# Optimization experiments

Measured on AMD Instinct MI355X. Metric: run time of the kernel, lower is better.

## Reference

```python
import jax, jax.numpy as jnp
import numpy as np

N = 4096     # num nodes
FEAT = 500   # knn attribute dim
HID = 512    # args.hid_dim
E = 65536    # edges (avg degree 16)
T = 8        # args.time -> euler steps with step_size=1


def setup_inputs() -> dict:
    key = jax.random.key(0)
    ks = jax.random.split(key, 10)
    knn = jax.random.normal(ks[0], (N, FEAT), jnp.float32)
    adj = jax.random.uniform(ks[1], (N, N), jnp.float32)
    norm_factor = jnp.ones((), jnp.float32)
    edge_index = jax.random.randint(ks[2], (2, E), 0, N, dtype=jnp.int32).astype(jnp.int64)
    edge_weight = jax.random.uniform(ks[3], (E,), jnp.float32)
    # AGCN params (init eye + small noise so math is non-trivial)
    w1 = jnp.eye(N, dtype=jnp.float32) + 0.01 * jax.random.normal(ks[4], (N, N), jnp.float32)
    w2 = jnp.eye(N, dtype=jnp.float32) + 0.01 * jax.random.normal(ks[5], (N, N), jnp.float32)
    # extractor: Linear(N, HID) then Linear(HID, HID), kaiming-normal (relu), zero bias
    W0 = jax.random.normal(ks[6], (HID, N), jnp.float32) * np.float32((2.0 / N) ** 0.5)
    b0 = jnp.zeros((HID,), jnp.float32)
    W1 = jax.random.normal(ks[7], (HID, HID), jnp.float32) * np.float32((2.0 / HID) ** 0.5)
    b1 = jnp.zeros((HID,), jnp.float32)
    # LaplacianODEFunc scalar params
    alpha_train = jnp.asarray(0.5, jnp.float32)
    beta_train = jnp.asarray(0.1, jnp.float32)
    return dict(knn=knn, adj=adj, norm_factor=norm_factor, w1=w1, w2=w2,
                W0=W0, b0=b0, W1=W1, b1=b1, edge_weight=edge_weight,
                alpha_train=alpha_train, beta_train=beta_train, edge_index=edge_index)


def _spmm(edge_index, edge_weight, x):
    # out[row] += w * x[col], row=edge_index[0], col=edge_index[1]
    msg = edge_weight[:, None] * x[edge_index[1]]          # [E, HID]
    return jax.ops.segment_sum(msg, edge_index[0], num_segments=x.shape[0])


def reference(knn, adj, norm_factor, w1, w2, W0, b0, W1, b1,
              edge_weight, alpha_train, beta_train, edge_index):
    # ---- AGCN ----
    H = (adj @ w1) @ adj.T                                  # [N, N]
    H = (H @ w2) @ knn                                      # [N, FEAT]
    embed = H @ H.T                                         # [N, N]
    norm = jnp.maximum(jnp.linalg.norm(embed, axis=1, keepdims=True), 1e-12)
    embed = embed / norm                                    # F.normalize(dim=1)
    # ---- extractor MLP (no activation in source; dropout=eval no-op) ----
    h = embed @ W0.T + b0                                   # [N, HID]
    h = h @ W1.T + b1                                       # [N, HID]
    # ---- ODE diffusion: dx/dt = sigmoid(a)*(Ax - x) + b*x0, explicit Euler dt=1 ----
    x0 = jax.lax.stop_gradient(h)
    alpha = jax.nn.sigmoid(alpha_train)

    def step(x, _):
        ax = _spmm(edge_index, edge_weight, x)
        return x + alpha * (ax - x) + beta_train * x0, None

    z_ode, _ = jax.lax.scan(step, h, None, length=T)
    z = jax.nn.relu(norm_factor * z_ode + h)
    z = (z - z.mean(0)) / jnp.std(z, ddof=1)                # torch std is unbiased
    return z
```

## Files before the change

### kernel.cpp

```cpp
#include <hip/hip_runtime.h>
#include <stdint.h>
#include <stddef.h>

typedef __bf16 bf16;
typedef __attribute__((ext_vector_type(8))) __bf16 bf16x8;
typedef __attribute__((ext_vector_type(4))) __bf16 bf16x4;
typedef __attribute__((ext_vector_type(4))) float f32x4;

#define NN 4096
#define HIDD 512
#define NE 65536

__device__ inline void gll16(const void* g, void* l) {
    __builtin_amdgcn_global_load_lds(
        (const __attribute__((address_space(1))) void*)g,
        (__attribute__((address_space(3))) void*)l, 16, 0, 0);
}

__global__ void cvt_f32_bf16(const float* __restrict__ in, bf16* __restrict__ out, int n) {
    int i = (blockIdx.x * 256 + threadIdx.x) * 4;
    if (i >= n) return;
    float4 v = *reinterpret_cast<const float4*>(in + i);
    bf16x4 o;
    o[0] = (bf16)v.x; o[1] = (bf16)v.y; o[2] = (bf16)v.z; o[3] = (bf16)v.w;
    *reinterpret_cast<bf16x4*>(out + i) = o;
}

__global__ void reduce_bf16_slices(const bf16* __restrict__ in, bf16* __restrict__ out,
                                   int n, int S) {
    int i = (blockIdx.x * 256 + threadIdx.x) * 8;
    if (i >= n) return;
    float acc[8] = {};
    for (int k = 0; k < S; ++k) {
        bf16x8 v = *reinterpret_cast<const bf16x8*>(in + (size_t)k * n + i);
#pragma unroll
        for (int j = 0; j < 8; ++j) acc[j] += (float)v[j];
    }
    bf16x8 o;
#pragma unroll
    for (int j = 0; j < 8; ++j) o[j] = (bf16)acc[j];
    *reinterpret_cast<bf16x8*>(out + i) = o;
}

__global__ void transpose_pad_f32(const float* __restrict__ in, bf16* __restrict__ out,
                                  int R, int C, int Cpad) {
    __shared__ bf16 tile[32][33];
    int c0 = blockIdx.x * 32, r0 = blockIdx.y * 32;
    int tx = threadIdx.x, ty = threadIdx.y;
    for (int i = ty; i < 32; i += 8) {
        int r = r0 + i, c = c0 + tx;
        bf16 v = (bf16)0.f;
        if (r < R && c < C) v = (bf16)in[(size_t)r * C + c];
        tile[i][tx] = v;
    }
    __syncthreads();
    for (int i = ty; i < 32; i += 8) {
        int oc = c0 + i, orow = r0 + tx;
        if (oc < Cpad && orow < R) out[(size_t)oc * R + orow] = tile[tx][i];
    }
}

__global__ void transpose_dual_f32(const float* __restrict__ in, bf16* __restrict__ outT,
                                   bf16* __restrict__ outD, int Nn) {
    __shared__ bf16 tile[32][33];
    int c0 = blockIdx.x * 32, r0 = blockIdx.y * 32;
    int tx = threadIdx.x, ty = threadIdx.y;
    for (int i = ty; i < 32; i += 8) {
        int r = r0 + i, c = c0 + tx;
        bf16 v = (bf16)in[(size_t)r * Nn + c];
        tile[i][tx] = v;
        outD[(size_t)r * Nn + c] = v;
    }
    __syncthreads();
    for (int i = ty; i < 32; i += 8)
        outT[(size_t)(c0 + i) * Nn + r0 + tx] = tile[tx][i];
}

__global__ void transpose_bf16(const bf16* __restrict__ in, bf16* __restrict__ out,
                               int R, int C) {
    __shared__ bf16 tile[32][33];
    int c0 = blockIdx.x * 32, r0 = blockIdx.y * 32;
    int tx = threadIdx.x, ty = threadIdx.y;
    for (int i = ty; i < 32; i += 8)
        tile[i][tx] = in[(size_t)(r0 + i) * C + c0 + tx];
    __syncthreads();
    for (int i = ty; i < 32; i += 8)
        out[(size_t)(c0 + i) * R + r0 + tx] = tile[tx][i];
}

template<int OMODE, bool HAS_BIAS, bool ROW_SCALE>
__global__ __launch_bounds__(256)
void gemm_nt(const bf16* __restrict__ A, const bf16* __restrict__ B,
             void* __restrict__ Cp, const float* __restrict__ bias,
             const float* __restrict__ rowscale, int M, int N, int K) {
    __shared__ __align__(16) bf16 As[128 * 32];
    __shared__ __align__(16) bf16 Bs[128 * 32];
    const int tid  = threadIdx.x;
    const int wave = tid >> 6;
    const int lane = tid & 63;
    const int m0 = blockIdx.y * 128, n0 = blockIdx.x * 128;
    const int lrow = lane >> 2;
    const int lcol = (lane & 3) * 8;
    const int c0 = wave * 2;
    const size_t arow0 = (size_t)(m0 + c0 * 16 + lrow) * K + lcol;
    const size_t arow1 = (size_t)(m0 + (c0 + 1) * 16 + lrow) * K + lcol;
    const size_t brow0 = (size_t)(n0 + c0 * 16 + lrow) * K + lcol;
    const size_t brow1 = (size_t)(n0 + (c0 + 1) * 16 + lrow) * K + lcol;
    bf16* asd0 = &As[c0 * 512];
    bf16* asd1 = &As[(c0 + 1) * 512];
    bf16* bsd0 = &Bs[c0 * 512];
    bf16* bsd1 = &Bs[(c0 + 1) * 512];

    f32x4 acc[4][4] = {};

    const int wm = (wave >> 1) * 64;
    const int wn = (wave & 1) * 64;
    const int fm = wm + (lane & 15);
    const int fn = wn + (lane & 15);
    const int fk = (lane >> 4) * 8;

    const int kper = K / gridDim.z;
    const int kz0 = blockIdx.z * kper;
    const int kz1 = kz0 + kper;

    for (int k0 = kz0; k0 < kz1; k0 += 32) {
        gll16(A + arow0 + k0, asd0);
        gll16(A + arow1 + k0, asd1);
        gll16(B + brow0 + k0, bsd0);
        gll16(B + brow1 + k0, bsd1);
        __syncthreads();
        bf16x8 af[4], bg[4];
#pragma unroll
        for (int i = 0; i < 4; ++i)
            af[i] = *reinterpret_cast<const bf16x8*>(&As[(fm + i * 16) * 32 + fk]);
#pragma unroll
        for (int j = 0; j < 4; ++j)
            bg[j] = *reinterpret_cast<const bf16x8*>(&Bs[(fn + j * 16) * 32 + fk]);
#pragma unroll
        for (int i = 0; i < 4; ++i)
#pragma unroll
            for (int j = 0; j < 4; ++j)
                acc[i][j] = __builtin_amdgcn_mfma_f32_16x16x32_bf16(af[i], bg[j], acc[i][j], 0, 0, 0);
        __syncthreads();
    }

    const int rbase = m0 + wm + (lane >> 4) * 4;
    const int cbase = n0 + wn + (lane & 15);
    float* outf = (float*)Cp + (size_t)blockIdx.z * M * N;
    bf16*  outb = (bf16*)Cp;
    bf16*  outp = (bf16*)Cp + (size_t)blockIdx.z * M * N;
#pragma unroll
    for (int i = 0; i < 4; ++i) {
#pragma unroll
        for (int j = 0; j < 4; ++j) {
            int col = cbase + j * 16;
            float bv = 0.f;
            if (HAS_BIAS) bv = bias[col];
#pragma unroll
            for (int r = 0; r < 4; ++r) {
                int row = rbase + i * 16 + r;
                float v = acc[i][j][r];
                if (ROW_SCALE) v *= rowscale[row];
                v += bv;
                if (OMODE == 0)      outf[(size_t)row * N + col] = v;
                else if (OMODE == 1) outb[(size_t)row * N + col] = (bf16)v;
                else                 outp[(size_t)row * N + col] = (bf16)v;
            }
        }
    }
}

__global__ void colnorm_part(const bf16* __restrict__ Ht, const float* __restrict__ Rf,
                             float* __restrict__ n2) {
    int i = blockIdx.x * 128 + threadIdx.x;
    int a0 = blockIdx.y * 64;
    const float* Rf2 = Rf + (size_t)HIDD * NN;
    float s = 0.f;
    for (int a = a0; a < a0 + 64; ++a) {
        size_t idx = (size_t)a * NN + i;
        s += (Rf[idx] + Rf2[idx]) * (float)Ht[idx];
    }
    atomicAdd(&n2[i], s);
}

__global__ void colnorm_fin(const float* __restrict__ n2, float* __restrict__ inv) {
    int i = blockIdx.x * 256 + threadIdx.x;
    inv[i] = 1.f / fmaxf(sqrtf(n2[i]), 1e-12f);
}

__global__ void bias_fuse(const float* __restrict__ W1, const float* __restrict__ b0,
                          const float* __restrict__ b1, float* __restrict__ bp) {
    int row = blockIdx.x * 4 + (threadIdx.x >> 6);
    int lane = threadIdx.x & 63;
    const float4* wr = (const float4*)(W1 + (size_t)row * HIDD);
    const float4* bz = (const float4*)b0;
    float s = 0.f;
#pragma unroll
    for (int j = 0; j < 2; ++j) {
        float4 a = wr[lane * 2 + j], b = bz[lane * 2 + j];
        s += a.x * b.x + a.y * b.y + a.z * b.z + a.w * b.w;
    }
    for (int off = 32; off; off >>= 1) s += __shfl_down(s, off);
    if (lane == 0) bp[row] = b1[row] + s;
}

__global__ void reduce2_scale_bias(const bf16* __restrict__ p, bf16* __restrict__ out,
                                   const float* __restrict__ inv, const float* __restrict__ bp) {
    int i = (blockIdx.x * 256 + threadIdx.x) * 8;
    const int n = NN * HIDD;
    bf16x8 a = *reinterpret_cast<const bf16x8*>(p + i);
    bf16x8 b = *reinterpret_cast<const bf16x8*>(p + n + i);
    int row = i >> 9;
    int col = i & (HIDD - 1);
    float sc = inv[row];
    bf16x8 o;
#pragma unroll
    for (int j = 0; j < 8; ++j)
        o[j] = (bf16)(((float)a[j] + (float)b[j]) * sc + bp[col + j]);
    *reinterpret_cast<bf16x8*>(out + i) = o;
}

__global__ void csr_count(const int* __restrict__ ei, int* __restrict__ cnt, int E) {
    int e = blockIdx.x * 256 + threadIdx.x;
    if (e < E) atomicAdd(&cnt[ei[e]], 1);
}

__global__ void scan_4096(const int* __restrict__ cnt, int* __restrict__ rs) {
    __shared__ int s[1024];
    int t = threadIdx.x;
    int b = t * 4;
    int a0 = cnt[b], a1 = cnt[b + 1], a2 = cnt[b + 2], a3 = cnt[b + 3];
    int tot = a0 + a1 + a2 + a3;
    s[t] = tot;
    __syncthreads();
    for (int off = 1; off < 1024; off <<= 1) {
        int v = (t >= off) ? s[t - off] : 0;
        __syncthreads();
        s[t] += v;
        __syncthreads();
    }
    int excl = s[t] - tot;
    rs[b] = excl; rs[b + 1] = excl + a0; rs[b + 2] = excl + a0 + a1; rs[b + 3] = excl + a0 + a1 + a2;
    if (t == 1023) rs[4096] = s[1023];
}

__global__ void csr_scatter(const int* __restrict__ ei, const float* __restrict__ ew,
                            int* __restrict__ cur, int* __restrict__ ccol,
                            float* __restrict__ cw, int E) {
    int e = blockIdx.x * 256 + threadIdx.x;
    if (e < E) {
        int r = ei[e];
        int p = atomicAdd(&cur[r], 1);
        ccol[p] = ei[E + e];
        cw[p] = ew[e];
    }
}

__global__ void ode_step_bf16(const bf16* __restrict__ xin, const bf16* __restrict__ x0,
                              bf16* __restrict__ xout, const int* __restrict__ rs,
                              const int* __restrict__ ccol, const float* __restrict__ cw,
                              const float* __restrict__ alpha_p, const float* __restrict__ beta_p) {
    int row = blockIdx.x * 4 + (threadIdx.x >> 6);
    int lane = threadIdx.x & 63;
    float alpha = 1.f / (1.f + expf(-alpha_p[0]));
    float beta = beta_p[0];
    const bf16x8* xin8 = (const bf16x8*)xin;
    float acc[8] = {};
    int p0 = rs[row], p1 = rs[row + 1];
    for (int p = p0; p < p1; ++p) {
        int c = ccol[p]; float w = cw[p];
        bf16x8 v = xin8[(size_t)c * 64 + lane];
#pragma unroll
        for (int j = 0; j < 8; ++j) acc[j] += w * (float)v[j];
    }
    bf16x8 xi = xin8[(size_t)row * 64 + lane];
    bf16x8 xz = ((const bf16x8*)x0)[(size_t)row * 64 + lane];
    bf16x8 r;
#pragma unroll
    for (int j = 0; j < 8; ++j) {
        float x = (float)xi[j];
        r[j] = (bf16)(x + alpha * (acc[j] - x) + beta * (float)xz[j]);
    }
    ((bf16x8*)xout)[(size_t)row * 64 + lane] = r;
}

__global__ void epi1(const bf16* __restrict__ x8, const bf16* __restrict__ h,
                     const float* __restrict__ nf_p, float* __restrict__ z,
                     float* __restrict__ colsum, float* __restrict__ gst) {
    __shared__ float r1[512], r2[512];
    int b = blockIdx.x, j = threadIdx.x;
    float nf = nf_p[0];
    float cp = 0.f, sq = 0.f;
    for (int i = 0; i < 8; ++i) {
        size_t idx = (size_t)(b * 8 + i) * HIDD + j;
        float v = nf * (float)x8[idx] + (float)h[idx];
        v = fmaxf(v, 0.f);
        z[idx] = v;
        cp += v; sq += v * v;
    }
    atomicAdd(&colsum[j], cp);
    r1[j] = cp; r2[j] = sq;
    __syncthreads();
    for (int off = 256; off > 0; off >>= 1) {
        if (j < off) { r1[j] += r1[j + off]; r2[j] += r2[j + off]; }
        __syncthreads();
    }
    if (j == 0) { atomicAdd(&gst[0], r1[0]); atomicAdd(&gst[1], r2[0]); }
}

__global__ void epi2(const float* __restrict__ z, const float* __restrict__ colsum,
                     const float* __restrict__ gst, float* __restrict__ out) {
    size_t idx = (size_t)blockIdx.x * 256 + threadIdx.x;
    int j = (int)(idx & (HIDD - 1));
    float n = (float)NN * (float)HIDD;
    float gmean = gst[0] / n;
    float var = (gst[1] - n * gmean * gmean) / (n - 1.f);
    float istd = rsqrtf(var);
    float mean = colsum[j] * (1.f / (float)NN);
    out[idx] = (z[idx] - mean) * istd;
}

extern "C" void kernel_launch(void* const* d_in, const int* in_sizes, int n_in,
                              void* d_out, int out_size, void* d_ws, size_t ws_size,
                              hipStream_t stream) {
    const float* knn  = (const float*)d_in[0];
    const float* adj  = (const float*)d_in[1];
    const float* nf   = (const float*)d_in[2];
    const float* w1   = (const float*)d_in[3];
    const float* w2   = (const float*)d_in[4];
    const float* W0   = (const float*)d_in[5];
    const float* b0   = (const float*)d_in[6];
    const float* W1   = (const float*)d_in[7];
    const float* b1   = (const float*)d_in[8];
    const float* ew   = (const float*)d_in[9];
    const float* alph = (const float*)d_in[10];
    const float* beta = (const float*)d_in[11];
    const int*   ei   = (const int*)d_in[12];

    char* w = (char*)d_ws;
    size_t off = 0;
    auto alloc = [&](size_t bytes) -> char* {
        char* p = w + off;
        off += (bytes + 255) & ~(size_t)255;
        return p;
    };
    const size_t SZ_NN  = (size_t)NN * NN * sizeof(bf16);
    const size_t SZ_TH  = (size_t)HIDD * NN * sizeof(bf16);
    bf16* Bar  = (bf16*)alloc(SZ_NN);
    bf16* Car  = (bf16*)alloc(SZ_NN);
    bf16* Adjb = (bf16*)alloc(SZ_NN);
    bf16* knnT = (bf16*)alloc(SZ_TH);
    bf16* tA   = (bf16*)alloc(SZ_TH);
    bf16* tB   = (bf16*)alloc(SZ_TH);
    float* tf  = (float*)alloc((size_t)32 * 1024 * 1024);
    bf16* Hm   = (bf16*)alloc(SZ_TH);
    bf16* Gb   = (bf16*)alloc((size_t)HIDD * HIDD * sizeof(bf16));
    bf16* M0b  = (bf16*)alloc((size_t)HIDD * HIDD * sizeof(bf16));
    bf16* Qtb  = (bf16*)alloc((size_t)HIDD * HIDD * sizeof(bf16));
    bf16* hb   = (bf16*)alloc((size_t)NN * HIDD * sizeof(bf16));
    float* inv = (float*)alloc(NN * sizeof(float));
    float* n2  = (float*)alloc(NN * sizeof(float));
    int*  cnt  = (int*)alloc(NN * sizeof(int));
    int*  rs   = (int*)alloc((NN + 1) * sizeof(int));
    int*  cur  = (int*)alloc(NN * sizeof(int));
    int*  ccol = (int*)alloc(NE * sizeof(int));
    float* cw  = (float*)alloc(NE * sizeof(float));
    float* colsum = (float*)alloc(HIDD * sizeof(float));
    float* gst = (float*)alloc(2 * sizeof(float));
    float* bp  = (float*)alloc(HIDD * sizeof(float));
    bf16* tfb = (bf16*)tf;
    bf16* W1b = (bf16*)((char*)Car + 16 * 1024 * 1024);
    bf16* xA  = (bf16*)Car;
    bf16* xB  = (bf16*)Car + (size_t)NN * HIDD;
    (void)ws_size; (void)n_in; (void)in_sizes; (void)out_size;

    dim3 tb(32, 8);
    const int nTH = HIDD * NN;
    const int nHH = HIDD * HIDD;

    transpose_pad_f32<<<dim3(16, 128), tb, 0, stream>>>(knn, knnT, NN, 500, HIDD);
    cvt_f32_bf16<<<(NN * NN) / 1024, 256, 0, stream>>>(w2, Car, NN * NN);
    transpose_dual_f32<<<dim3(128, 128), tb, 0, stream>>>(adj, Bar, Adjb, NN);

    gemm_nt<2, false, false><<<dim3(32, 4, 8), 256, 0, stream>>>(knnT, Car, tfb, nullptr, nullptr, HIDD, NN, NN);
    reduce_bf16_slices<<<nTH / 2048, 256, 0, stream>>>(tfb, tA, nTH, 8);
    gemm_nt<2, false, false><<<dim3(32, 4, 8), 256, 0, stream>>>(tA, Bar, tfb, nullptr, nullptr, HIDD, NN, NN);
    reduce_bf16_slices<<<nTH / 2048, 256, 0, stream>>>(tfb, tB, nTH, 8);
    cvt_f32_bf16<<<(NN * NN) / 1024, 256, 0, stream>>>(w1, Car, NN * NN);
    gemm_nt<2, false, false><<<dim3(32, 4, 8), 256, 0, stream>>>(tB, Car, tfb, nullptr, nullptr, HIDD, NN, NN);
    reduce_bf16_slices<<<nTH / 2048, 256, 0, stream>>>(tfb, tA, nTH, 8);
    gemm_nt<2, false, false><<<dim3(32, 4, 8), 256, 0, stream>>>(tA, Adjb, tfb, nullptr, nullptr, HIDD, NN, NN);
    reduce_bf16_slices<<<nTH / 2048, 256, 0, stream>>>(tfb, tB, nTH, 8);

    transpose_bf16<<<dim3(128, 16), tb, 0, stream>>>(tB, Hm, HIDD, NN);

    gemm_nt<2, false, false><<<dim3(4, 4, 32), 256, 0, stream>>>(tB, tB, tfb, nullptr, nullptr, HIDD, HIDD, NN);
    reduce_bf16_slices<<<nHH / 2048, 256, 0, stream>>>(tfb, Gb, nHH, 32);

    gemm_nt<0, false, false><<<dim3(32, 4, 2), 256, 0, stream>>>(Gb, Hm, tf, nullptr, nullptr, HIDD, NN, HIDD);
    hipMemsetAsync(n2, 0, NN * sizeof(float), stream);
    colnorm_part<<<dim3(32, 8), 128, 0, stream>>>(tB, tf, n2);
    colnorm_fin<<<NN / 256, 256, 0, stream>>>(n2, inv);

    cvt_f32_bf16<<<(HIDD * NN) / 1024, 256, 0, stream>>>(W0, Car, HIDD * NN);
    gemm_nt<2, false, false><<<dim3(4, 4, 32), 256, 0, stream>>>(tB, Car, tfb, nullptr, nullptr, HIDD, HIDD, NN);
    reduce_bf16_slices<<<nHH / 2048, 256, 0, stream>>>(tfb, M0b, nHH, 32);

    cvt_f32_bf16<<<(HIDD * HIDD) / 1024, 256, 0, stream>>>(W1, W1b, HIDD * HIDD);
    gemm_nt<2, false, false><<<dim3(4, 4, 8), 256, 0, stream>>>(W1b, M0b, tfb, nullptr, nullptr, HIDD, HIDD, HIDD);
    reduce_bf16_slices<<<nHH / 2048, 256, 0, stream>>>(tfb, Qtb, nHH, 8);

    bias_fuse<<<128, 256, 0, stream>>>(W1, b0, b1, bp);

    gemm_nt<2, false, false><<<dim3(4, 32, 2), 256, 0, stream>>>(Hm, Qtb, tfb, nullptr, nullptr, NN, HIDD, HIDD);
    reduce2_scale_bias<<<(NN * HIDD) / 2048, 256, 0, stream>>>(tfb, hb, inv, bp);

    hipMemsetAsync(cnt, 0, NN * sizeof(int), stream);
    csr_count<<<NE / 256, 256, 0, stream>>>(ei, cnt, NE);
    scan_4096<<<1, 1024, 0, stream>>>(cnt, rs);
    hipMemcpyAsync(cur, rs, NN * sizeof(int), hipMemcpyDeviceToDevice, stream);
    csr_scatter<<<NE / 256, 256, 0, stream>>>(ei, ew, cur, ccol, cw, NE);

    const bf16* xi = hb;
    bf16* xo = xA;
    for (int s = 0; s < 8; ++s) {
        ode_step_bf16<<<NN / 4, 256, 0, stream>>>(xi, hb, xo, rs, ccol, cw, alph, beta);
        xi = xo;
        xo = (s % 2 == 0) ? xB : xA;
    }

    hipMemsetAsync(colsum, 0, HIDD * sizeof(float), stream);
    hipMemsetAsync(gst, 0, 2 * sizeof(float), stream);
    epi1<<<NN / 8, 512, 0, stream>>>(xB, hb, nf, tf, colsum, gst);
    epi2<<<(NN * HIDD) / 256, 256, 0, stream>>>(tf, colsum, gst, (float*)d_out);
}
```

Before: 694.1 us.

## Triple-buffer GEMM LDS loads, vectorize adjacency transpose, halve split-K

The GEMM main loop now keeps three shared-memory buffers. Tiles are issued two iterations ahead using async global-to-LDS loads and vmcnt waits, which replaces the two barriers per k-step with a single one so that loads overlap MFMA work. The adjacency transpose/convert kernel moves to 64x64 tiles with float4 loads and 8-wide bf16 stores. The four big N×N chained GEMMs go from 8 to 4 split-K slices, which cuts partial-sum traffic and reduce work but also halves grid parallelism; tripled LDS use may lower occupancy.

```diff
diff --git a/kernel.cpp b/kernel.cpp
--- a/kernel.cpp
+++ b/kernel.cpp
@@ -62,18 +62,31 @@
 
 __global__ void transpose_dual_f32(const float* __restrict__ in, bf16* __restrict__ outT,
                                    bf16* __restrict__ outD, int Nn) {
-    __shared__ bf16 tile[32][33];
-    int c0 = blockIdx.x * 32, r0 = blockIdx.y * 32;
-    int tx = threadIdx.x, ty = threadIdx.y;
-    for (int i = ty; i < 32; i += 8) {
-        int r = r0 + i, c = c0 + tx;
-        bf16 v = (bf16)in[(size_t)r * Nn + c];
-        tile[i][tx] = v;
-        outD[(size_t)r * Nn + c] = v;
+    __shared__ bf16 tile[64][68];
+    int r0 = blockIdx.y * 64, c0 = blockIdx.x * 64;
+    int t = threadIdx.x;
+    int tx = t & 15;
+    int ty = t >> 4;
+#pragma unroll
+    for (int i = 0; i < 4; ++i) {
+        int r = ty + i * 16;
+        float4 v = *reinterpret_cast<const float4*>(in + (size_t)(r0 + r) * Nn + c0 + tx * 4);
+        bf16x4 o;
+        o[0] = (bf16)v.x; o[1] = (bf16)v.y; o[2] = (bf16)v.z; o[3] = (bf16)v.w;
+        *reinterpret_cast<bf16x4*>(&tile[r][tx * 4]) = o;
+        *reinterpret_cast<bf16x4*>(outD + (size_t)(r0 + r) * Nn + c0 + tx * 4) = o;
     }
     __syncthreads();
-    for (int i = ty; i < 32; i += 8)
-        outT[(size_t)(c0 + i) * Nn + r0 + tx] = tile[tx][i];
+    int c = t >> 2;
+    int rs = (t & 3) * 16;
+#pragma unroll
+    for (int j = 0; j < 2; ++j) {
+        int r = rs + j * 8;
+        bf16x8 o;
+#pragma unroll
+        for (int e = 0; e < 8; ++e) o[e] = tile[r + e][c];
+        *reinterpret_cast<bf16x8*>(outT + (size_t)(c0 + c) * Nn + r0 + r) = o;
+    }
 }
 
 __global__ void transpose_bf16(const bf16* __restrict__ in, bf16* __restrict__ out,
@@ -93,8 +106,8 @@
 void gemm_nt(const bf16* __restrict__ A, const bf16* __restrict__ B,
              void* __restrict__ Cp, const float* __restrict__ bias,
              const float* __restrict__ rowscale, int M, int N, int K) {
-    __shared__ __align__(16) bf16 As[128 * 32];
-    __shared__ __align__(16) bf16 Bs[128 * 32];
+    __shared__ __align__(16) bf16 As[3][128 * 32];
+    __shared__ __align__(16) bf16 Bs[3][128 * 32];
     const int tid  = threadIdx.x;
     const int wave = tid >> 6;
     const int lane = tid & 63;
@@ -106,10 +119,6 @@
     const size_t arow1 = (size_t)(m0 + (c0 + 1) * 16 + lrow) * K + lcol;
     const size_t brow0 = (size_t)(n0 + c0 * 16 + lrow) * K + lcol;
     const size_t brow1 = (size_t)(n0 + (c0 + 1) * 16 + lrow) * K + lcol;
-    bf16* asd0 = &As[c0 * 512];
-    bf16* asd1 = &As[(c0 + 1) * 512];
-    bf16* bsd0 = &Bs[c0 * 512];
-    bf16* bsd1 = &Bs[(c0 + 1) * 512];
 
     f32x4 acc[4][4] = {};
 
@@ -121,27 +130,41 @@
 
     const int kper = K / gridDim.z;
     const int kz0 = blockIdx.z * kper;
-    const int kz1 = kz0 + kper;
-
-    for (int k0 = kz0; k0 < kz1; k0 += 32) {
-        gll16(A + arow0 + k0, asd0);
-        gll16(A + arow1 + k0, asd1);
-        gll16(B + brow0 + k0, bsd0);
-        gll16(B + brow1 + k0, bsd1);
-        __syncthreads();
+    const int nt = kper >> 5;
+
+    auto stage = [&](int t, int buf) {
+        const int k0 = kz0 + (t << 5);
+        gll16(A + arow0 + k0, &As[buf][c0 * 512]);
+        gll16(A + arow1 + k0, &As[buf][(c0 + 1) * 512]);
+        gll16(B + brow0 + k0, &Bs[buf][c0 * 512]);
+        gll16(B + brow1 + k0, &Bs[buf][(c0 + 1) * 512]);
+    };
+
+    stage(0, 0);
+    if (nt > 1) stage(1, 1);
+
+    int cur = 0;
+    for (int t = 0; t < nt; ++t) {
+        if (t + 1 < nt) asm volatile("s_waitcnt vmcnt(4)" ::: "memory");
+        else            asm volatile("s_waitcnt vmcnt(0)" ::: "memory");
+        __builtin_amdgcn_s_barrier();
+        if (t + 2 < nt) {
+            int nb = cur + 2; if (nb >= 3) nb -= 3;
+            stage(t + 2, nb);
+        }
         bf16x8 af[4], bg[4];
 #pragma unroll
         for (int i = 0; i < 4; ++i)
-            af[i] = *reinterpret_cast<const bf16x8*>(&As[(fm + i * 16) * 32 + fk]);
+            af[i] = *reinterpret_cast<const bf16x8*>(&As[cur][(fm + i * 16) * 32 + fk]);
 #pragma unroll
         for (int j = 0; j < 4; ++j)
-            bg[j] = *reinterpret_cast<const bf16x8*>(&Bs[(fn + j * 16) * 32 + fk]);
+            bg[j] = *reinterpret_cast<const bf16x8*>(&Bs[cur][(fn + j * 16) * 32 + fk]);
 #pragma unroll
         for (int i = 0; i < 4; ++i)
 #pragma unroll
             for (int j = 0; j < 4; ++j)
                 acc[i][j] = __builtin_amdgcn_mfma_f32_16x16x32_bf16(af[i], bg[j], acc[i][j], 0, 0, 0);
-        __syncthreads();
+        cur = (cur + 1 == 3) ? 0 : cur + 1;
     }
 
     const int rbase = m0 + wm + (lane >> 4) * 4;
@@ -380,17 +403,17 @@
 
     transpose_pad_f32<<<dim3(16, 128), tb, 0, stream>>>(knn, knnT, NN, 500, HIDD);
     cvt_f32_bf16<<<(NN * NN) / 1024, 256, 0, stream>>>(w2, Car, NN * NN);
-    transpose_dual_f32<<<dim3(128, 128), tb, 0, stream>>>(adj, Bar, Adjb, NN);
-
-    gemm_nt<2, false, false><<<dim3(32, 4, 8), 256, 0, stream>>>(knnT, Car, tfb, nullptr, nullptr, HIDD, NN, NN);
-    reduce_bf16_slices<<<nTH / 2048, 256, 0, stream>>>(tfb, tA, nTH, 8);
-    gemm_nt<2, false, false><<<dim3(32, 4, 8), 256, 0, stream>>>(tA, Bar, tfb, nullptr, nullptr, HIDD, NN, NN);
-    reduce_bf16_slices<<<nTH / 2048, 256, 0, stream>>>(tfb, tB, nTH, 8);
+    transpose_dual_f32<<<dim3(64, 64), 256, 0, stream>>>(adj, Bar, Adjb, NN);
+
+    gemm_nt<2, false, false><<<dim3(32, 4, 4), 256, 0, stream>>>(knnT, Car, tfb, nullptr, nullptr, HIDD, NN, NN);
+    reduce_bf16_slices<<<nTH / 2048, 256, 0, stream>>>(tfb, tA, nTH, 4);
+    gemm_nt<2, false, false><<<dim3(32, 4, 4), 256, 0, stream>>>(tA, Bar, tfb, nullptr, nullptr, HIDD, NN, NN);
+    reduce_bf16_slices<<<nTH / 2048, 256, 0, stream>>>(tfb, tB, nTH, 4);
     cvt_f32_bf16<<<(NN * NN) / 1024, 256, 0, stream>>>(w1, Car, NN * NN);
-    gemm_nt<2, false, false><<<dim3(32, 4, 8), 256, 0, stream>>>(tB, Car, tfb, nullptr, nullptr, HIDD, NN, NN);
-    reduce_bf16_slices<<<nTH / 2048, 256, 0, stream>>>(tfb, tA, nTH, 8);
-    gemm_nt<2, false, false><<<dim3(32, 4, 8), 256, 0, stream>>>(tA, Adjb, tfb, nullptr, nullptr, HIDD, NN, NN);
-    reduce_bf16_slices<<<nTH / 2048, 256, 0, stream>>>(tfb, tB, nTH, 8);
+    gemm_nt<2, false, false><<<dim3(32, 4, 4), 256, 0, stream>>>(tB, Car, tfb, nullptr, nullptr, HIDD, NN, NN);
+    reduce_bf16_slices<<<nTH / 2048, 256, 0, stream>>>(tfb, tA, nTH, 4);
+    gemm_nt<2, false, false><<<dim3(32, 4, 4), 256, 0, stream>>>(tA, Adjb, tfb, nullptr, nullptr, HIDD, NN, NN);
+    reduce_bf16_slices<<<nTH / 2048, 256, 0, stream>>>(tfb, tB, nTH, 4);
 
     transpose_bf16<<<dim3(128, 16), tb, 0, stream>>>(tB, Hm, HIDD, NN);
 
```

Result: faster. 648.8 us (-6.5%).
